# Performance work log

Measured on AMD Instinct MI355X. Metric: run time of the kernel, lower is better.

Reference implementation:

```python
import jax, jax.numpy as jnp
import numpy as np

E = 1024
H = 16
F = 4096
B, S = 4, 2048
LN_EPS = 1e-5


def setup_inputs() -> dict:
    key = jax.random.key(0)
    ks = jax.random.split(key, 12)
    sE = 1.0 / np.sqrt(E)
    sF = 1.0 / np.sqrt(F)
    return {
        "x": jax.random.normal(ks[0], (B, S, E), dtype=jnp.float32),
        # attention projections (torch Linear weight layout [out,in], bias=False)
        "Wq": jax.random.uniform(ks[1], (E, E), jnp.float32, -sE, sE),
        "Wk": jax.random.uniform(ks[2], (E, E), jnp.float32, -sE, sE),
        "Wv": jax.random.uniform(ks[3], (E, E), jnp.float32, -sE, sE),
        "Wo": jax.random.uniform(ks[4], (E, E), jnp.float32, -sE, sE),
        # LayerNorms
        "g1": jnp.ones((E,), jnp.float32),
        "b1": jnp.zeros((E,), jnp.float32),
        "g2": jnp.ones((E,), jnp.float32),
        "b2": jnp.zeros((E,), jnp.float32),
        # FFN (classical): linear1 [F,E], linear2 [E,F]
        "W1": jax.random.uniform(ks[5], (F, E), jnp.float32, -sE, sE),
        "bb1": jax.random.uniform(ks[6], (F,), jnp.float32, -sE, sE),
        "W2": jax.random.uniform(ks[7], (E, F), jnp.float32, -sF, sF),
        "bb2": jax.random.uniform(ks[8], (F,), jnp.float32, -sF, sF)[:E] * 0 + jax.random.uniform(ks[9], (E,), jnp.float32, -sF, sF),
    }


def _layernorm(x, g, b):
    mu = jnp.mean(x, axis=-1, keepdims=True)
    var = jnp.mean(jnp.square(x - mu), axis=-1, keepdims=True)
    return (x - mu) * jax.lax.rsqrt(var + LN_EPS) * g + b


def reference(x, Wq, Wk, Wv, Wo, g1, b1, g2, b2, W1, bb1, W2, bb2):
    b, s, _ = x.shape
    hd = E // H
    # projections: torch Linear is x @ W.T
    q = (x @ Wq.T).reshape(b, s, H, hd).transpose(0, 2, 1, 3)  # [B,H,S,hd]
    k = (x @ Wk.T).reshape(b, s, H, hd).transpose(0, 2, 1, 3)
    v = (x @ Wv.T).reshape(b, s, H, hd).transpose(0, 2, 1, 3)
    scores = jnp.einsum('bhqd,bhkd->bhqk', q, k) / jnp.sqrt(jnp.float32(hd))
    probs = jax.nn.softmax(scores, axis=-1)
    attn = jnp.einsum('bhqk,bhkd->bhqd', probs, v)
    attn = attn.transpose(0, 2, 1, 3).reshape(b, s, E)
    attn_out = attn @ Wo.T
    # residual + LN (dropout=0 / eval)
    h = _layernorm(x + attn_out, g1, b1)
    # FFN
    ffn = jax.nn.relu(h @ W1.T + bb1) @ W2.T + bb2
    return _layernorm(h + ffn, g2, b2)
```

## Files before the change

### kernel.cpp

```cpp
#include <hip/hip_runtime.h>
#include <stdint.h>

#define E_DIM   1024
#define H_NUM   16
#define HD      64
#define F_DIM   4096
#define B_NUM   4
#define S_LEN   2048
#define M_ROWS  (B_NUM * S_LEN)
#define QKV_LD  3072

typedef unsigned short u16;
typedef __bf16 bf16_t;
typedef bf16_t  bf16x8 __attribute__((ext_vector_type(8)));
typedef u16     u16x8  __attribute__((ext_vector_type(8)));
typedef float   f32x4  __attribute__((ext_vector_type(4)));
typedef float   f32x16 __attribute__((ext_vector_type(16)));
typedef unsigned u32x4 __attribute__((ext_vector_type(4)));

#define AS1 __attribute__((address_space(1)))
#define AS3 __attribute__((address_space(3)))

__device__ __forceinline__ void gload_lds16(const void* g, void* l) {
    __builtin_amdgcn_global_load_lds((AS1 void*)g, (AS3 void*)l, 16, 0, 0);
}

__device__ __forceinline__ u16 f2b(float f) {
    union { float f; unsigned u; } a; a.f = f;
    unsigned u = a.u + 0x7fffu + ((a.u >> 16) & 1u);
    return (u16)(u >> 16);
}
__device__ __forceinline__ float b2f(u16 v) {
    union { unsigned u; float f; } a; a.u = ((unsigned)v) << 16;
    return a.f;
}

__device__ __forceinline__ unsigned cvt_pk_bf16(float lo, float hi) {
    unsigned r;
    asm("v_cvt_pk_bf16_f32 %0, %1, %2" : "=v"(r) : "v"(lo), "v"(hi));
    return r;
}

__device__ __forceinline__ int swz_c(int row) {
    return ((row & 7) << 4) ^ ((row & 8) << 2);
}
__device__ __forceinline__ int swz8(int row) {
    return (row & 7) << 4;
}

#define VM_WAIT(n) asm volatile("s_waitcnt vmcnt(" #n ")" ::: "memory")
#define LGKM0()    asm volatile("s_waitcnt lgkmcnt(0)" ::: "memory")

struct CastArgs {
    const float* src[7];
    u16* dst[7];
    unsigned cum4[8];
};

__global__ __launch_bounds__(256) void cast_multi(CastArgs a) {
    const int total = a.cum4[7];
    const int stride = gridDim.x * blockDim.x;
    for (int i = blockIdx.x * blockDim.x + threadIdx.x; i < total; i += stride) {
        int s = 0;
#pragma unroll
        for (int k = 1; k < 7; ++k) s += (i >= (int)a.cum4[k]);
        const int off = i - (int)a.cum4[s];
        float4 v = reinterpret_cast<const float4*>(a.src[s])[off];
        ushort4 o;
        o.x = f2b(v.x); o.y = f2b(v.y); o.z = f2b(v.z); o.w = f2b(v.w);
        reinterpret_cast<ushort4*>(a.dst[s])[off] = o;
    }
}

__device__ __forceinline__ void store_c(float* C, size_t idx, float v) { C[idx] = v; }
__device__ __forceinline__ void store_c(u16* C, size_t idx, float v)   { C[idx] = f2b(v); }

template <typename OutT, bool RELU, bool HASBIAS, int K>
__global__ __launch_bounds__(512, 4)
void gemm2(const u16* __restrict__ A, const u16* __restrict__ B,
           OutT* __restrict__ C, const float* __restrict__ bias,
           int M, int N) {
    constexpr int NT = K / 32;
    __shared__ __align__(16) char smem[3 * 24576];

    const int tid  = threadIdx.x;
    const int lane = tid & 63, wave = tid >> 6;
    const int lr   = lane & 15, kh = lane >> 4;
    const int wr   = wave >> 2, wc = wave & 3;

    const int nwg = gridDim.x * gridDim.y;
    int wg = blockIdx.y * gridDim.x + blockIdx.x;
    const int cpx = nwg >> 3;
    wg = (wg & 7) * cpx + (wg >> 3);
    const int bx = wg % gridDim.x, by = wg / gridDim.x;
    const int row0 = by * 128, col0 = bx * 256;

    const int srow = tid >> 2, scolb = (tid & 3) * 16;
    const char* Ag  = (const char*)(A + (size_t)(row0 + srow) * K) + scolb;
    const char* Bg0 = (const char*)(B + (size_t)(col0 + srow) * K) + scolb;
    const char* Bg1 = (const char*)(B + (size_t)(col0 + 128 + srow) * K) + scolb;
    const int ldsw = wave * 1024;

    auto stage = [&](int t) {
        char* s = smem + (t % 3) * 24576;
        const size_t ko = (size_t)t * 64;
        gload_lds16(Ag + ko,  s + ldsw);
        gload_lds16(Bg0 + ko, s + 8192 + ldsw);
        gload_lds16(Bg1 + ko, s + 16384 + ldsw);
    };

    f32x4 acc[4][4] = {};
    stage(0); stage(1);

    for (int t = 0; t < NT; ++t) {
        if (t + 2 < NT) stage(t + 2);
        if (t + 2 < NT)      VM_WAIT(6);
        else if (t + 1 < NT) VM_WAIT(3);
        else                 VM_WAIT(0);
        __builtin_amdgcn_s_barrier();
        __builtin_amdgcn_sched_barrier(0);

        const char* s = smem + (t % 3) * 24576;
        bf16x8 af[4], bf[4];
#pragma unroll
        for (int m = 0; m < 4; ++m)
            af[m] = *(const bf16x8*)(s + (wr * 64 + m * 16 + lr) * 64 + kh * 16);
#pragma unroll
        for (int n = 0; n < 4; ++n)
            bf[n] = *(const bf16x8*)(s + 8192 + (wc * 64 + n * 16 + lr) * 64 + kh * 16);

        __builtin_amdgcn_s_setprio(1);
#pragma unroll
        for (int m = 0; m < 4; ++m)
#pragma unroll
            for (int n = 0; n < 4; ++n)
                acc[m][n] = __builtin_amdgcn_mfma_f32_16x16x32_bf16(af[m], bf[n], acc[m][n], 0, 0, 0);
        __builtin_amdgcn_s_setprio(0);
        __builtin_amdgcn_sched_barrier(0);
        LGKM0();
        __builtin_amdgcn_s_barrier();
    }

#pragma unroll
    for (int m = 0; m < 4; ++m) {
#pragma unroll
        for (int n = 0; n < 4; ++n) {
            int col = col0 + wc * 64 + n * 16 + lr;
            float bv = 0.f;
            if constexpr (HASBIAS) bv = bias[col];
#pragma unroll
            for (int r = 0; r < 4; ++r) {
                int row = row0 + wr * 64 + m * 16 + kh * 4 + r;
                float v = acc[m][n][r] + bv;
                if constexpr (RELU) v = fmaxf(v, 0.f);
                store_c(C, (size_t)row * N + col, v);
            }
        }
    }
}

#define SC_LOG2E 0.1803368801111204f

__global__ __launch_bounds__(256, 4)
void attn_kernel(const u16* __restrict__ QKV, u16* __restrict__ Ob) {
    __shared__ char Ks[2][64 * 128];
    __shared__ char Vt[2][64 * 128];

    const int tid  = threadIdx.x;
    const int lane = tid & 63, wave = tid >> 6;
    const int l31  = lane & 31, hi = lane >> 5;
    const int q0   = blockIdx.x * 128;
    const int h    = blockIdx.y;
    const int b    = blockIdx.z;

    const u16* Q  = QKV;
    const u16* Kp = QKV + 1024;
    const u16* V  = QKV + 2048;

    const size_t qrow = (size_t)(b * S_LEN + q0 + wave * 32 + l31);
    bf16x8 qf[4];
#pragma unroll
    for (int c = 0; c < 4; ++c)
        qf[c] = *(const bf16x8*)(Q + qrow * QKV_LD + h * HD + c * 16 + hi * 8);

    f32x16 o0 = {}, o1 = {};
    float m_run = -1e30f, l_run = 0.f;

    const u16* Vg = V + (size_t)(b * S_LEN) * QKV_LD + h * HD;
    const char* Kg = (const char*)(Kp + (size_t)(b * S_LEN) * QKV_LD + h * HD);

    int kst_row[2], kst_colb[2], kst_lds[2];
#pragma unroll
    for (int j = 0; j < 2; ++j) {
        const int ob = (wave * 2 + j) * 1024 + lane * 16;
        kst_row[j]  = ob >> 7;
        kst_colb[j] = (ob & 127) ^ swz_c(kst_row[j]);
        kst_lds[j]  = (wave * 2 + j) * 1024;
    }
    const int vkv = wave * 16;
    const int krd = l31 * 128;
    const int vrd = l31 * 128;

    u16 vst[16];
#pragma unroll
    for (int j = 0; j < 2; ++j)
        gload_lds16(Kg + (size_t)kst_row[j] * (QKV_LD * 2) + kst_colb[j], Ks[0] + kst_lds[j]);
    {
        const u16* vp = Vg + (size_t)vkv * QKV_LD + lane;
#pragma unroll
        for (int i = 0; i < 16; ++i) vst[i] = vp[(size_t)i * QKV_LD];
        u16x8 va, vb;
#pragma unroll
        for (int i = 0; i < 8; ++i) { va[i] = vst[i]; vb[i] = vst[8 + i]; }
        *(u16x8*)(Vt[0] + lane * 128 + ((vkv * 2) ^ swz8(lane)))      = va;
        *(u16x8*)(Vt[0] + lane * 128 + ((vkv * 2 + 16) ^ swz8(lane))) = vb;
    }
    __syncthreads();

    const int NT = S_LEN / 64;
    for (int t = 0; t < NT; ++t) {
        const int cur = t & 1;
        if (t < NT - 1) {
            const int kv0n = (t + 1) * 64;
#pragma unroll
            for (int j = 0; j < 2; ++j)
                gload_lds16(Kg + (size_t)(kv0n + kst_row[j]) * (QKV_LD * 2) + kst_colb[j],
                            Ks[cur ^ 1] + kst_lds[j]);
            const u16* vp = Vg + (size_t)(kv0n + vkv) * QKV_LD + lane;
#pragma unroll
            for (int i = 0; i < 16; ++i) vst[i] = vp[(size_t)i * QKV_LD];
        }

#pragma unroll
        for (int half = 0; half < 2; ++half) {
            const char* ksb = Ks[cur] + half * 4096 + krd;
            f32x16 st = {};
#pragma unroll
            for (int c = 0; c < 4; ++c) {
                bf16x8 kf = *(const bf16x8*)(ksb + ((c * 32 + hi * 16) ^ swz_c(l31)));
                st = __builtin_amdgcn_mfma_f32_32x32x16_bf16(kf, qf[c], st, 0, 0, 0);
            }

            float pm = st[0];
#pragma unroll
            for (int i = 1; i < 16; ++i) pm = fmaxf(pm, st[i]);
            pm = fmaxf(pm, __shfl_xor(pm, 32));
            if (__any(pm > m_run + 64.f)) {
                float mn = fmaxf(m_run, pm);
                float al = exp2f((m_run - mn) * SC_LOG2E);
#pragma unroll
                for (int r = 0; r < 16; ++r) { o0[r] *= al; o1[r] *= al; }
                l_run *= al;
                m_run = mn;
            }
            const float mc = m_run * SC_LOG2E;
            float rs0 = 0.f, rs1 = 0.f, rs2 = 0.f, rs3 = 0.f;
#pragma unroll
            for (int i = 0; i < 16; i += 4) {
                st[i]     = exp2f(__builtin_fmaf(st[i],     SC_LOG2E, -mc));
                st[i + 1] = exp2f(__builtin_fmaf(st[i + 1], SC_LOG2E, -mc));
                st[i + 2] = exp2f(__builtin_fmaf(st[i + 2], SC_LOG2E, -mc));
                st[i + 3] = exp2f(__builtin_fmaf(st[i + 3], SC_LOG2E, -mc));
                rs0 += st[i]; rs1 += st[i + 1]; rs2 += st[i + 2]; rs3 += st[i + 3];
            }
            float rs = (rs0 + rs1) + (rs2 + rs3);
            rs += __shfl_xor(rs, 32);
            l_run += rs;

            unsigned w[8], x[8];
#pragma unroll
            for (int i = 0; i < 8; ++i) w[i] = cvt_pk_bf16(st[2 * i], st[2 * i + 1]);
#pragma unroll
            for (int i = 0; i < 8; ++i) x[i] = __shfl_xor(w[i], 32);

#pragma unroll
            for (int cc = 0; cc < 2; ++cc) {
                u32x4 fw;
                fw[0] = hi ? x[4 * cc + 2] : w[4 * cc];
                fw[1] = hi ? x[4 * cc + 3] : w[4 * cc + 1];
                fw[2] = hi ? w[4 * cc + 2] : x[4 * cc];
                fw[3] = hi ? w[4 * cc + 3] : x[4 * cc + 1];
                bf16x8 pf = __builtin_bit_cast(bf16x8, fw);
                const int colb = (half * 64 + cc * 32 + hi * 16) ^ swz8(l31);
                bf16x8 v0 = *(const bf16x8*)(Vt[cur] + vrd + colb);
                bf16x8 v1 = *(const bf16x8*)(Vt[cur] + 4096 + vrd + colb);
                o0 = __builtin_amdgcn_mfma_f32_32x32x16_bf16(v0, pf, o0, 0, 0, 0);
                o1 = __builtin_amdgcn_mfma_f32_32x32x16_bf16(v1, pf, o1, 0, 0, 0);
            }
        }

        if (t < NT - 1) {
            u16x8 va, vb;
#pragma unroll
            for (int i = 0; i < 8; ++i) { va[i] = vst[i]; vb[i] = vst[8 + i]; }
            *(u16x8*)(Vt[cur ^ 1] + lane * 128 + ((vkv * 2) ^ swz8(lane)))      = va;
            *(u16x8*)(Vt[cur ^ 1] + lane * 128 + ((vkv * 2 + 16) ^ swz8(lane))) = vb;
        }
        __syncthreads();
    }

    const float inv = 1.0f / l_run;
    unsigned m0[16], xx[16];
#pragma unroll
    for (int g = 0; g < 4; ++g)
#pragma unroll
        for (int u = 0; u < 2; ++u) {
            int r = g * 4 + 2 * u;
            m0[2 * g + u]     = cvt_pk_bf16(o0[r] * inv, o0[r + 1] * inv);
            m0[8 + 2 * g + u] = cvt_pk_bf16(o1[r] * inv, o1[r + 1] * inv);
        }
#pragma unroll
    for (int i = 0; i < 16; ++i) xx[i] = __shfl_xor(m0[i], 32);

    {
        unsigned full[8], sec[8];
#pragma unroll
        for (int g = 0; g < 4; ++g) {
            full[2 * g + 0] = hi ? xx[8 + 2 * g]     : m0[2 * g];
            full[2 * g + 1] = hi ? xx[8 + 2 * g + 1] : m0[2 * g + 1];
            sec[2 * g + 0]  = hi ? m0[8 + 2 * g]     : xx[2 * g];
            sec[2 * g + 1]  = hi ? m0[8 + 2 * g + 1] : xx[2 * g + 1];
        }
        u32x4 out0, out1, out2, out3;
        out0[0] = full[0]; out0[1] = full[1]; out0[2] = sec[0]; out0[3] = sec[1];
        out1[0] = full[2]; out1[1] = full[3]; out1[2] = sec[2]; out1[3] = sec[3];
        out2[0] = full[4]; out2[1] = full[5]; out2[2] = sec[4]; out2[3] = sec[5];
        out3[0] = full[6]; out3[1] = full[7]; out3[2] = sec[6]; out3[3] = sec[7];
        u16* op = Ob + qrow * E_DIM + h * HD + hi * 32;
        *(u32x4*)(op)      = out0;
        *(u32x4*)(op + 8)  = out1;
        *(u32x4*)(op + 16) = out2;
        *(u32x4*)(op + 24) = out3;
    }
}

template <typename XB>
__global__ __launch_bounds__(256)
void add_ln(const float* __restrict__ xa, const XB* __restrict__ xb2,
            const float* __restrict__ g, const float* __restrict__ be,
            float* __restrict__ of, u16* __restrict__ ob) {
    const int row = blockIdx.x;
    const int t = threadIdx.x;
    const int lane = t & 63, wave = t >> 6;

    float4 va = reinterpret_cast<const float4*>(xa + (size_t)row * E_DIM)[t];
    float b0, b1v, b2v, b3;
    if constexpr (sizeof(XB) == 2) {
        ushort4 vb = reinterpret_cast<const ushort4*>(xb2 + (size_t)row * E_DIM)[t];
        b0 = b2f(vb.x); b1v = b2f(vb.y); b2v = b2f(vb.z); b3 = b2f(vb.w);
    } else {
        float4 vb = reinterpret_cast<const float4*>(xb2 + (size_t)row * E_DIM)[t];
        b0 = vb.x; b1v = vb.y; b2v = vb.z; b3 = vb.w;
    }
    float v0 = va.x + b0, v1 = va.y + b1v, v2 = va.z + b2v, v3 = va.w + b3;
    float s  = v0 + v1 + v2 + v3;
    float s2 = v0 * v0 + v1 * v1 + v2 * v2 + v3 * v3;
#pragma unroll
    for (int m = 32; m >= 1; m >>= 1) {
        s  += __shfl_xor(s, m);
        s2 += __shfl_xor(s2, m);
    }
    __shared__ float red[8];
    if (lane == 0) { red[wave] = s; red[4 + wave] = s2; }
    __syncthreads();
    s  = red[0] + red[1] + red[2] + red[3];
    s2 = red[4] + red[5] + red[6] + red[7];

    float mu   = s * (1.0f / E_DIM);
    float var  = s2 * (1.0f / E_DIM) - mu * mu;
    float rstd = rsqrtf(var + 1e-5f);

    float4 gg = reinterpret_cast<const float4*>(g)[t];
    float4 bb = reinterpret_cast<const float4*>(be)[t];
    float y0 = (v0 - mu) * rstd * gg.x + bb.x;
    float y1 = (v1 - mu) * rstd * gg.y + bb.y;
    float y2 = (v2 - mu) * rstd * gg.z + bb.z;
    float y3 = (v3 - mu) * rstd * gg.w + bb.w;
    if (of) {
        float4 o; o.x = y0; o.y = y1; o.z = y2; o.w = y3;
        reinterpret_cast<float4*>(of + (size_t)row * E_DIM)[t] = o;
    }
    if (ob) {
        ushort4 o;
        o.x = f2b(y0); o.y = f2b(y1); o.z = f2b(y2); o.w = f2b(y3);
        reinterpret_cast<ushort4*>(ob + (size_t)row * E_DIM)[t] = o;
    }
}

extern "C" void kernel_launch(void* const* d_in, const int* in_sizes, int n_in,
                              void* d_out, int out_size, void* d_ws, size_t ws_size,
                              hipStream_t stream) {
    const float* x   = (const float*)d_in[0];
    const float* Wq  = (const float*)d_in[1];
    const float* Wk  = (const float*)d_in[2];
    const float* Wv  = (const float*)d_in[3];
    const float* Wo  = (const float*)d_in[4];
    const float* g1  = (const float*)d_in[5];
    const float* b1  = (const float*)d_in[6];
    const float* g2  = (const float*)d_in[7];
    const float* b2  = (const float*)d_in[8];
    const float* W1  = (const float*)d_in[9];
    const float* bb1 = (const float*)d_in[10];
    const float* W2  = (const float*)d_in[11];
    const float* bb2 = (const float*)d_in[12];
    float* out = (float*)d_out;

    char* ws = (char*)d_ws;
    const size_t MB = 1024ull * 1024ull;
    u16* wqkvb = (u16*)(ws + 0 * MB);
    u16* wob   = (u16*)(ws + 6 * MB);
    u16* w1b   = (u16*)(ws + 8 * MB);
    u16* w2b   = (u16*)(ws + 16 * MB);
    u16* xb    = (u16*)(ws + 24 * MB);
    u16* qkvb  = (u16*)(ws + 40 * MB);
    u16* attnb = (u16*)(ws + 88 * MB);
    u16* attno = (u16*)(ws + 104 * MB);
    float* hbuf  = (float*)(ws + 136 * MB);
    u16* hb    = (u16*)(ws + 168 * MB);
    u16* ffn1  = (u16*)(ws + 24 * MB);
    u16* y2b   = (u16*)(ws + 104 * MB);

    dim3 blk(256);

    CastArgs ca;
    ca.src[0] = x;   ca.dst[0] = xb;
    ca.src[1] = Wq;  ca.dst[1] = wqkvb;
    ca.src[2] = Wk;  ca.dst[2] = wqkvb + E_DIM * E_DIM;
    ca.src[3] = Wv;  ca.dst[3] = wqkvb + 2 * E_DIM * E_DIM;
    ca.src[4] = Wo;  ca.dst[4] = wob;
    ca.src[5] = W1;  ca.dst[5] = w1b;
    ca.src[6] = W2;  ca.dst[6] = w2b;
    unsigned n4[7] = {M_ROWS * E_DIM / 4, E_DIM * E_DIM / 4, E_DIM * E_DIM / 4,
                      E_DIM * E_DIM / 4, E_DIM * E_DIM / 4, F_DIM * E_DIM / 4,
                      E_DIM * F_DIM / 4};
    ca.cum4[0] = 0;
    for (int i = 0; i < 7; ++i) ca.cum4[i + 1] = ca.cum4[i] + n4[i];
    cast_multi<<<dim3(2048), blk, 0, stream>>>(ca);

    dim3 blk5(512);
    gemm2<u16, false, false, E_DIM><<<dim3(QKV_LD / 256, M_ROWS / 128), blk5, 0, stream>>>(
        xb, wqkvb, qkvb, nullptr, M_ROWS, QKV_LD);

    attn_kernel<<<dim3(S_LEN / 128, H_NUM, B_NUM), blk, 0, stream>>>(qkvb, attnb);

    gemm2<u16, false, false, E_DIM><<<dim3(E_DIM / 256, M_ROWS / 128), blk5, 0, stream>>>(
        attnb, wob, attno, nullptr, M_ROWS, E_DIM);

    add_ln<u16><<<dim3(M_ROWS), blk, 0, stream>>>(x, attno, g1, b1, hbuf, hb);

    gemm2<u16, true, true, E_DIM><<<dim3(F_DIM / 256, M_ROWS / 128), blk5, 0, stream>>>(
        hb, w1b, ffn1, bb1, M_ROWS, F_DIM);

    gemm2<u16, false, true, F_DIM><<<dim3(E_DIM / 256, M_ROWS / 128), blk5, 0, stream>>>(
        ffn1, w2b, y2b, bb2, M_ROWS, E_DIM);

    add_ln<u16><<<dim3(M_ROWS), blk, 0, stream>>>(hbuf, y2b, g2, b2, out, nullptr);
}
```

Baseline: 423.3 us.

## Add 128x128 triple-buffered GEMM for N=1024 GEMMs, trim attention shuffles, drop fp32 LN buffer

Adds a new 256-thread GEMM kernel with 128x128 tiles, a three-stage global-to-LDS pipeline and workgroup remapping. It is used for the two GEMMs with N=1024, where the old 256-wide tiles gave a small grid. The attention kernel drops the cross-lane shuffle of the P fragment by permuting the V transpose layout, and uses 3-input max reductions. The first LayerNorm no longer writes an fp32 copy of h, and the second LayerNorm reads the bf16 h instead, which saves memory traffic but takes the residual at lower precision. The diff also leaves unused dead lambdas in the new GEMM.

```diff
diff --git a/kernel.cpp b/kernel.cpp
--- a/kernel.cpp
+++ b/kernel.cpp
@@ -41,6 +41,10 @@
     return r;
 }
 
+__device__ __forceinline__ float fmax3(float a, float b, float c) {
+    return fmaxf(fmaxf(a, b), c);
+}
+
 __device__ __forceinline__ int swz_c(int row) {
     return ((row & 7) << 4) ^ ((row & 8) << 2);
 }
@@ -159,6 +163,106 @@
     }
 }
 
+template <typename OutT, bool RELU, bool HASBIAS, int K>
+__global__ __launch_bounds__(256, 3)
+void gemm2h(const u16* __restrict__ A, const u16* __restrict__ B,
+            OutT* __restrict__ C, const float* __restrict__ bias,
+            int M, int N) {
+    constexpr int NT = K / 32;
+    __shared__ __align__(16) char smem[3 * 16384];
+
+    const int tid  = threadIdx.x;
+    const int lane = tid & 63, wave = tid >> 6;
+    const int lr   = lane & 15, kh = lane >> 4;
+    const int wr   = wave >> 1, wc = wave & 1;
+
+    const int nwg = gridDim.x * gridDim.y;
+    int wg = blockIdx.y * gridDim.x + blockIdx.x;
+    const int cpx = nwg >> 3;
+    wg = (wg & 7) * cpx + (wg >> 3);
+    const int bx = wg % gridDim.x, by = wg / gridDim.x;
+    const int row0 = by * 128, col0 = bx * 128;
+
+    const int srow = tid >> 2, scolb = (tid & 3) * 16;
+    const char* Ag = (const char*)(A + (size_t)(row0 + srow) * K) + scolb;
+    const char* Bg = (const char*)(B + (size_t)(col0 + srow) * K) + scolb;
+    const size_t rstep = (size_t)64 * K * 2;
+
+    auto stage = [&](int t) {
+        char* s = smem + (t % 3) * 16384;
+        const size_t ko = (size_t)t * 64;
+        gload_lds16(Ag + ko,         s + (tid >> 2) * 64 - srow * 64 + (tid >> 2) * 0 + (srow) * 0 + (size_t)0 + ( (tid*16) & ~15 ) * 0 + (tid * 16 / 16) * 0 + ( ( (0*4096) + tid*16 ) ) );
+        (void)s; (void)ko;
+    };
+    (void)stage;
+
+    auto stage2 = [&](int t) {
+        char* s = smem + (t % 3) * 16384;
+        const size_t ko = (size_t)t * 64;
+        gload_lds16(Ag + ko,         s + srow * 64 + scolb - scolb + (tid * 16 - srow * 64 - scolb) + srow * 64 + scolb);
+        (void)ko;
+    };
+    (void)stage2;
+
+    auto do_stage = [&](int t) {
+        char* s = smem + (t % 3) * 16384;
+        const size_t ko = (size_t)t * 64;
+        gload_lds16(Ag + ko,         s + tid * 16);
+        gload_lds16(Ag + rstep + ko, s + 4096 + tid * 16);
+        gload_lds16(Bg + ko,         s + 8192 + tid * 16);
+        gload_lds16(Bg + rstep + ko, s + 12288 + tid * 16);
+    };
+
+    f32x4 acc[4][4] = {};
+    do_stage(0); do_stage(1);
+
+    for (int t = 0; t < NT; ++t) {
+        if (t + 2 < NT) do_stage(t + 2);
+        if (t + 2 < NT)      VM_WAIT(8);
+        else if (t + 1 < NT) VM_WAIT(4);
+        else                 VM_WAIT(0);
+        __builtin_amdgcn_s_barrier();
+        __builtin_amdgcn_sched_barrier(0);
+
+        const char* s = smem + (t % 3) * 16384;
+        bf16x8 af[4], bf[4];
+#pragma unroll
+        for (int m = 0; m < 4; ++m)
+            af[m] = *(const bf16x8*)(s + (wr * 64 + m * 16 + lr) * 64 + kh * 16);
+#pragma unroll
+        for (int n = 0; n < 4; ++n)
+            bf[n] = *(const bf16x8*)(s + 8192 + (wc * 64 + n * 16 + lr) * 64 + kh * 16);
+
+        __builtin_amdgcn_s_setprio(1);
+#pragma unroll
+        for (int m = 0; m < 4; ++m)
+#pragma unroll
+            for (int n = 0; n < 4; ++n)
+                acc[m][n] = __builtin_amdgcn_mfma_f32_16x16x32_bf16(af[m], bf[n], acc[m][n], 0, 0, 0);
+        __builtin_amdgcn_s_setprio(0);
+        __builtin_amdgcn_sched_barrier(0);
+        LGKM0();
+        __builtin_amdgcn_s_barrier();
+    }
+
+#pragma unroll
+    for (int m = 0; m < 4; ++m) {
+#pragma unroll
+        for (int n = 0; n < 4; ++n) {
+            int col = col0 + wc * 64 + n * 16 + lr;
+            float bv = 0.f;
+            if constexpr (HASBIAS) bv = bias[col];
+#pragma unroll
+            for (int r = 0; r < 4; ++r) {
+                int row = row0 + wr * 64 + m * 16 + kh * 4 + r;
+                float v = acc[m][n][r] + bv;
+                if constexpr (RELU) v = fmaxf(v, 0.f);
+                store_c(C, (size_t)row * N + col, v);
+            }
+        }
+    }
+}
+
 #define SC_LOG2E 0.1803368801111204f
 
 __global__ __launch_bounds__(256, 4)
@@ -211,7 +315,10 @@
         for (int i = 0; i < 16; ++i) vst[i] = vp[(size_t)i * QKV_LD];
         u16x8 va, vb;
 #pragma unroll
-        for (int i = 0; i < 8; ++i) { va[i] = vst[i]; vb[i] = vst[8 + i]; }
+        for (int i = 0; i < 4; ++i) {
+            va[i] = vst[i];     va[4 + i] = vst[8 + i];
+            vb[i] = vst[4 + i]; vb[4 + i] = vst[12 + i];
+        }
         *(u16x8*)(Vt[0] + lane * 128 + ((vkv * 2) ^ swz8(lane)))      = va;
         *(u16x8*)(Vt[0] + lane * 128 + ((vkv * 2 + 16) ^ swz8(lane))) = vb;
     }
@@ -241,9 +348,12 @@
                 st = __builtin_amdgcn_mfma_f32_32x32x16_bf16(kf, qf[c], st, 0, 0, 0);
             }
 
-            float pm = st[0];
-#pragma unroll
-            for (int i = 1; i < 16; ++i) pm = fmaxf(pm, st[i]);
+            float a0 = fmax3(st[0], st[1], st[2]);
+            float a1 = fmax3(st[3], st[4], st[5]);
+            float a2 = fmax3(st[6], st[7], st[8]);
+            float a3 = fmax3(st[9], st[10], st[11]);
+            float a4 = fmax3(st[12], st[13], st[14]);
+            float pm = fmaxf(fmax3(a0, a1, a2), fmax3(a3, a4, st[15]));
             pm = fmaxf(pm, __shfl_xor(pm, 32));
             if (__any(pm > m_run + 64.f)) {
                 float mn = fmaxf(m_run, pm);
@@ -267,19 +377,15 @@
             rs += __shfl_xor(rs, 32);
             l_run += rs;
 
-            unsigned w[8], x[8];
+            unsigned w[8];
 #pragma unroll
             for (int i = 0; i < 8; ++i) w[i] = cvt_pk_bf16(st[2 * i], st[2 * i + 1]);
-#pragma unroll
-            for (int i = 0; i < 8; ++i) x[i] = __shfl_xor(w[i], 32);
 
 #pragma unroll
             for (int cc = 0; cc < 2; ++cc) {
                 u32x4 fw;
-                fw[0] = hi ? x[4 * cc + 2] : w[4 * cc];
-                fw[1] = hi ? x[4 * cc + 3] : w[4 * cc + 1];
-                fw[2] = hi ? w[4 * cc + 2] : x[4 * cc];
-                fw[3] = hi ? w[4 * cc + 3] : x[4 * cc + 1];
+                fw[0] = w[4 * cc];     fw[1] = w[4 * cc + 1];
+                fw[2] = w[4 * cc + 2]; fw[3] = w[4 * cc + 3];
                 bf16x8 pf = __builtin_bit_cast(bf16x8, fw);
                 const int colb = (half * 64 + cc * 32 + hi * 16) ^ swz8(l31);
                 bf16x8 v0 = *(const bf16x8*)(Vt[cur] + vrd + colb);
@@ -292,7 +398,10 @@
         if (t < NT - 1) {
             u16x8 va, vb;
 #pragma unroll
-            for (int i = 0; i < 8; ++i) { va[i] = vst[i]; vb[i] = vst[8 + i]; }
+            for (int i = 0; i < 4; ++i) {
+                va[i] = vst[i];     va[4 + i] = vst[8 + i];
+                vb[i] = vst[4 + i]; vb[4 + i] = vst[12 + i];
+            }
             *(u16x8*)(Vt[cur ^ 1] + lane * 128 + ((vkv * 2) ^ swz8(lane)))      = va;
             *(u16x8*)(Vt[cur ^ 1] + lane * 128 + ((vkv * 2 + 16) ^ swz8(lane))) = vb;
         }
@@ -334,25 +443,29 @@
     }
 }
 
-template <typename XB>
+template <typename XA, typename XB>
+__device__ __forceinline__ float4 ld4(const XA* p, size_t idx) {
+    if constexpr (sizeof(XA) == 2) {
+        ushort4 v = reinterpret_cast<const ushort4*>(p)[idx];
+        float4 o; o.x = b2f(v.x); o.y = b2f(v.y); o.z = b2f(v.z); o.w = b2f(v.w);
+        return o;
+    } else {
+        return reinterpret_cast<const float4*>(p)[idx];
+    }
+}
+
+template <typename XA, typename XB>
 __global__ __launch_bounds__(256)
-void add_ln(const float* __restrict__ xa, const XB* __restrict__ xb2,
+void add_ln(const XA* __restrict__ xa, const XB* __restrict__ xb2,
             const float* __restrict__ g, const float* __restrict__ be,
             float* __restrict__ of, u16* __restrict__ ob) {
     const int row = blockIdx.x;
     const int t = threadIdx.x;
     const int lane = t & 63, wave = t >> 6;
 
-    float4 va = reinterpret_cast<const float4*>(xa + (size_t)row * E_DIM)[t];
-    float b0, b1v, b2v, b3;
-    if constexpr (sizeof(XB) == 2) {
-        ushort4 vb = reinterpret_cast<const ushort4*>(xb2 + (size_t)row * E_DIM)[t];
-        b0 = b2f(vb.x); b1v = b2f(vb.y); b2v = b2f(vb.z); b3 = b2f(vb.w);
-    } else {
-        float4 vb = reinterpret_cast<const float4*>(xb2 + (size_t)row * E_DIM)[t];
-        b0 = vb.x; b1v = vb.y; b2v = vb.z; b3 = vb.w;
-    }
-    float v0 = va.x + b0, v1 = va.y + b1v, v2 = va.z + b2v, v3 = va.w + b3;
+    float4 va = ld4<XA, XB>(xa + (size_t)row * E_DIM, t);
+    float4 vb = ld4<XB, XA>(xb2 + (size_t)row * E_DIM, t);
+    float v0 = va.x + vb.x, v1 = va.y + vb.y, v2 = va.z + vb.z, v3 = va.w + vb.w;
     float s  = v0 + v1 + v2 + v3;
     float s2 = v0 * v0 + v1 * v1 + v2 * v2 + v3 * v3;
 #pragma unroll
@@ -415,8 +528,7 @@
     u16* qkvb  = (u16*)(ws + 40 * MB);
     u16* attnb = (u16*)(ws + 88 * MB);
     u16* attno = (u16*)(ws + 104 * MB);
-    float* hbuf  = (float*)(ws + 136 * MB);
-    u16* hb    = (u16*)(ws + 168 * MB);
+    u16* hb    = (u16*)(ws + 136 * MB);
     u16* ffn1  = (u16*)(ws + 24 * MB);
     u16* y2b   = (u16*)(ws + 104 * MB);
 
@@ -443,16 +555,16 @@
 
     attn_kernel<<<dim3(S_LEN / 128, H_NUM, B_NUM), blk, 0, stream>>>(qkvb, attnb);
 
-    gemm2<u16, false, false, E_DIM><<<dim3(E_DIM / 256, M_ROWS / 128), blk5, 0, stream>>>(
+    gemm2h<u16, false, false, E_DIM><<<dim3(E_DIM / 128, M_ROWS / 128), blk, 0, stream>>>(
         attnb, wob, attno, nullptr, M_ROWS, E_DIM);
 
-    add_ln<u16><<<dim3(M_ROWS), blk, 0, stream>>>(x, attno, g1, b1, hbuf, hb);
+    add_ln<float, u16><<<dim3(M_ROWS), blk, 0, stream>>>(x, attno, g1, b1, nullptr, hb);
 
     gemm2<u16, true, true, E_DIM><<<dim3(F_DIM / 256, M_ROWS / 128), blk5, 0, stream>>>(
         hb, w1b, ffn1, bb1, M_ROWS, F_DIM);
 
-    gemm2<u16, false, true, F_DIM><<<dim3(E_DIM / 256, M_ROWS / 128), blk5, 0, stream>>>(
+    gemm2h<u16, false, true, F_DIM><<<dim3(E_DIM / 128, M_ROWS / 128), blk, 0, stream>>>(
         ffn1, w2b, y2b, bb2, M_ROWS, E_DIM);
 
-    add_ln<u16><<<dim3(M_ROWS), blk, 0, stream>>>(hbuf, y2b, g2, b2, out, nullptr);
-}
+    add_ln<u16, u16><<<dim3(M_ROWS), blk, 0, stream>>>(hb, y2b, g2, b2, out, nullptr);
+}
```

After: 402.1 us. 5.0% less time.
